# Kernel optimization log

Measured on AMD Instinct MI355X. Metric: run time of the kernel, lower is better.

Reference implementation:

```python
import jax, jax.numpy as jnp
import numpy as np
import math

H = 1024          # hidden_size
NUM_LAYERS = 2
V = 32000         # target vocabulary
S = 4096          # source length
W = 64            # window_size
WIN = 2 * W + 1   # max window width (static)
H2 = math.ceil(H / 2)
STD_SQ = (W / 2) ** 2
NEG = -1e30


def setup_inputs() -> dict:
    key = jax.random.key(0)
    ks = jax.random.split(key, 16)
    s = 0.02
    return {
        "source_sentence_length": S,
        "encoder_output": jax.random.normal(ks[0], (S, 1, H), jnp.float32),
        "word": jax.random.randint(ks[1], (1, 1), 0, V),
        "h0": jnp.zeros((NUM_LAYERS, 1, H), jnp.float32),
        "c0": jnp.zeros((NUM_LAYERS, 1, H), jnp.float32),
        "embedding": jax.random.normal(ks[2], (V, H), jnp.float32) * s,
        "lstm_w_ih": jax.random.normal(ks[3], (NUM_LAYERS, 4 * H, H), jnp.float32) * s,
        "lstm_w_hh": jax.random.normal(ks[4], (NUM_LAYERS, 4 * H, H), jnp.float32) * s,
        "lstm_b_ih": jax.random.normal(ks[5], (NUM_LAYERS, 4 * H), jnp.float32) * s,
        "lstm_b_hh": jax.random.normal(ks[6], (NUM_LAYERS, 4 * H), jnp.float32) * s,
        "att_fc1_w": jax.random.normal(ks[7], (H2, H), jnp.float32) * s,
        "att_fc1_b": jax.random.normal(ks[8], (H2,), jnp.float32) * s,
        "att_fc2_w": jax.random.normal(ks[9], (1, H2), jnp.float32) * s,
        "att_fc2_b": jax.random.normal(ks[10], (1,), jnp.float32) * s,
        "fc1_w": jax.random.normal(ks[11], (H, 2 * H), jnp.float32) * s,
        "fc1_b": jax.random.normal(ks[12], (H,), jnp.float32) * s,
        "fc2_w": jax.random.normal(ks[13], (V, H), jnp.float32) * s,
        "fc2_b": jax.random.normal(ks[14], (V,), jnp.float32) * s,
    }


def reference(source_sentence_length, encoder_output, word, h0, c0, embedding,
              lstm_w_ih, lstm_w_hh, lstm_b_ih, lstm_b_hh,
              att_fc1_w, att_fc1_b, att_fc2_w, att_fc2_b,
              fc1_w, fc1_b, fc2_w, fc2_b):
    Sf = jnp.float32(source_sentence_length)
    # embedding lookup (seq=1, batch=1) -> (H,)
    x = embedding[word[0, 0]]
    # stacked LSTM, single time step, torch gate order i,f,g,o
    h_list, c_list = [], []
    for l in range(NUM_LAYERS):
        gates = x @ lstm_w_ih[l].T + lstm_b_ih[l] + h0[l, 0] @ lstm_w_hh[l].T + lstm_b_hh[l]
        i, f, g, o = jnp.split(gates, 4)
        c_new = jax.nn.sigmoid(f) * c0[l, 0] + jax.nn.sigmoid(i) * jnp.tanh(g)
        h_new = jax.nn.sigmoid(o) * jnp.tanh(c_new)
        h_list.append(h_new); c_list.append(c_new)
        x = h_new
    h_n = jnp.stack(h_list)[:, None, :]  # (L,1,H)
    c_n = jnp.stack(c_list)[:, None, :]
    h_t = x  # (H,) decoder output at this step
    # ---- dynamic Gaussian-windowed attention ----
    p = Sf * jax.nn.sigmoid(jnp.tanh(h_t @ att_fc1_w.T + att_fc1_b) @ att_fc2_w.T + att_fc2_b)
    p = p.reshape(())
    ws = jnp.round(jnp.clip(p - W, 0, None)).astype(jnp.int32)                      # clamp(min=0)
    we = jnp.round(jnp.clip(p + W, None, source_sentence_length - 1)).astype(jnp.int32)  # clamp(max=S-1)
    idx = ws + jnp.arange(WIN, dtype=jnp.int32)          # fixed-width window
    valid = idx <= we                                    # replicates [ws:we+1] slice
    h_s = encoder_output[jnp.clip(idx, 0, source_sentence_length - 1), 0, :]
    scores = jnp.where(valid, h_s @ h_t, NEG)
    a = jax.nn.softmax(scores)                           # softmax over window
    gauss = jnp.exp((idx.astype(jnp.float32) - p) / (2.0 * STD_SQ))
    a = jnp.where(valid, a * gauss, 0.0)
    ctx = a @ h_s                                        # (H,)
    # ---- output MLP ----
    out = jnp.tanh(jnp.concatenate([ctx, h_t]) @ fc1_w.T + fc1_b)
    y = jax.nn.log_softmax(out @ fc2_w.T + fc2_b)
    return (y.reshape(1, 1, V), out.reshape(1, 1, H), h_n, c_n, a.reshape(1, 1, WIN))
```

## Files before the change

kernel.cpp:

```cpp
#include <hip/hip_runtime.h>

#define HDIM 1024
#define VD   32000
#define WINN 129
#define NEGV (-1e30f)

#define X_     0
#define HT_    1024
#define G_     5120
#define ATT1_  9216
#define CAT_   9728
#define PARTM_ 12000
#define PARTS_ 13000
#define LOG_   16384

#define O_Y   0
#define O_OUT 32000
#define O_HN  33024
#define O_CN  35072
#define O_A   37120

__device__ __forceinline__ float wred(float v){
  #pragma unroll
  for(int off=32; off; off>>=1) v += __shfl_xor(v, off, 64);
  return v;
}
__device__ __forceinline__ float wmax(float v){
  #pragma unroll
  for(int off=32; off; off>>=1) v = fmaxf(v, __shfl_xor(v, off, 64));
  return v;
}
__device__ __forceinline__ float sigf(float x){ return 1.f/(1.f+expf(-x)); }
__device__ __forceinline__ float dot4(float4 a, float4 b){
  return a.x*b.x + a.y*b.y + a.z*b.z + a.w*b.w;
}
__device__ __forceinline__ float4 ld4(const float* p){ return *(const float4*)p; }


__global__ __launch_bounds__(256) void k_lstm0(
    const float* __restrict__ wih, const float* __restrict__ whh,
    const float* __restrict__ bih, const float* __restrict__ bhh,
    const int* __restrict__ word, const float* __restrict__ emb,
    const float* __restrict__ h0, const float* __restrict__ c0,
    float* __restrict__ ws, float* __restrict__ hn, float* __restrict__ cn){
  int j = blockIdx.x*4 + (threadIdx.x>>6);
  int lane = threadIdx.x & 63;
  const float* x    = emb + ((size_t)word[0]<<10);
  const float* h00  = h0;
  const float* h01  = h0 + HDIM;
  const float* wih0 = wih + ((size_t)j<<10);
  const float* whh0 = whh + ((size_t)j<<10);
  const float* whh1 = whh + ((size_t)(4096 + j)<<10);
  float acc[12];
  #pragma unroll
  for (int g=0; g<12; g++) acc[g]=0.f;
  #pragma unroll
  for (int c=0;c<4;c++){
    int o = lane*4 + 256*c;
    float4 xv = ld4(x+o), av = ld4(h00+o), bv = ld4(h01+o);
    #pragma unroll
    for (int g=0; g<4; g++){
      acc[g]   += dot4(ld4(wih0 + ((size_t)g<<20) + o), xv);
      acc[4+g] += dot4(ld4(whh0 + ((size_t)g<<20) + o), av);
      acc[8+g] += dot4(ld4(whh1 + ((size_t)g<<20) + o), bv);
    }
  }
  #pragma unroll
  for (int g=0; g<12; g++) acc[g] = wred(acc[g]);
  if (lane==0){
    float gi = acc[0]+acc[4] + bih[j]      + bhh[j];
    float gf = acc[1]+acc[5] + bih[1024+j] + bhh[1024+j];
    float gg = acc[2]+acc[6] + bih[2048+j] + bhh[2048+j];
    float go = acc[3]+acc[7] + bih[3072+j] + bhh[3072+j];
    float cc = sigf(gf)*c0[j] + sigf(gi)*tanhf(gg);
    float hh = sigf(go)*tanhf(cc);
    ws[X_+j] = hh; hn[j]=hh; cn[j]=cc;
    #pragma unroll
    for (int g=0; g<4; g++)
      ws[G_ + g*1024 + j] = acc[8+g] + bih[4096 + g*1024 + j] + bhh[4096 + g*1024 + j];
  }
}

__global__ __launch_bounds__(256) void k_lstm1(
    const float* __restrict__ wih1, const float* __restrict__ c0l,
    float* __restrict__ ws, float* __restrict__ hn, float* __restrict__ cn){
  int j = blockIdx.x*4 + (threadIdx.x>>6);
  int lane = threadIdx.x & 63;
  const float* wr = wih1 + ((size_t)j<<10);
  float acc[4] = {0.f,0.f,0.f,0.f};
  #pragma unroll
  for (int c=0;c<4;c++){
    int o = lane*4 + 256*c;
    float4 hv = ld4(ws + X_ + o);
    #pragma unroll
    for (int g=0; g<4; g++)
      acc[g] += dot4(ld4(wr + ((size_t)g<<20) + o), hv);
  }
  #pragma unroll
  for (int g=0; g<4; g++) acc[g]=wred(acc[g]);
  if (lane==0){
    float gi = acc[0] + ws[G_ + j];
    float gf = acc[1] + ws[G_ + 1024 + j];
    float gg = acc[2] + ws[G_ + 2048 + j];
    float go = acc[3] + ws[G_ + 3072 + j];
    float cc = sigf(gf)*c0l[j] + sigf(gi)*tanhf(gg);
    float hh = sigf(go)*tanhf(cc);
    ws[HT_+j]=hh; ws[CAT_+HDIM+j]=hh; hn[j]=hh; cn[j]=cc;
  }
}

__global__ __launch_bounds__(256) void k_att1(const float* __restrict__ w,
    const float* __restrict__ b, float* __restrict__ ws){
  int gid = blockIdx.x*256 + threadIdx.x;
  int r = gid >> 6, lane = gid & 63;
  const float* wr = w + ((size_t)r<<10);
  float acc = 0.f;
  #pragma unroll
  for (int j=0; j<4; j++){
    int o = lane*4 + 256*j;
    acc += dot4(ld4(wr+o), ld4(ws+HT_+o));
  }
  acc = wred(acc);
  if (lane==0) ws[ATT1_ + r] = tanhf(acc + b[r]);
}

__global__ __launch_bounds__(1024) void k_attn(const float* __restrict__ enc,
    const int* __restrict__ slen, const float* __restrict__ a2w,
    const float* __restrict__ a2b, float* __restrict__ ws, float* __restrict__ aout){
  __shared__ float sarr[WINN];
  __shared__ float av[WINN];
  __shared__ int   ci[WINN];
  __shared__ float red[2];
  __shared__ float pinfo[1];
  __shared__ int   iw[2];
  int t = threadIdx.x, lane = t & 63, wv = t >> 6;
  float Sf = (float)slen[0];
  int smax = slen[0]-1;
  if (wv==0){
    float pacc = 0.f;
    #pragma unroll
    for (int c=0;c<2;c++){
      int o = lane*4 + 256*c;
      pacc += dot4(ld4(a2w+o), ld4(ws+ATT1_+o));
    }
    pacc = wred(pacc);
    float p = Sf * sigf(pacc + a2b[0]);
    if (t==0){
      pinfo[0] = p;
      iw[0] = (int)rintf(fmaxf(p-64.f,0.f));
      iw[1] = (int)rintf(fminf(p+64.f, Sf-1.f));
    }
  }
  __syncthreads();
  float p = pinfo[0];
  int wsi = iw[0], wei = iw[1];
  for (int k = wv; k < WINN; k += 16){
    int idx = wsi + k;
    int c = idx > smax ? smax : idx;
    const float* er = enc + ((size_t)c<<10);
    float acc=0.f;
    #pragma unroll
    for (int cc=0;cc<4;cc++){
      int o = lane*4 + 256*cc;
      acc += dot4(ld4(er+o), ld4(ws+HT_+o));
    }
    acc = wred(acc);
    if (lane==0){
      sarr[k] = (idx<=wei)? acc : NEGV;
      ci[k] = c;
    }
  }
  __syncthreads();
  if (t < 64){
    float m = fmaxf(sarr[t], sarr[t+64]);
    if (t==0) m = fmaxf(m, sarr[128]);
    m = wmax(m);
    if (t==0) red[0]=m;
  }
  __syncthreads();
  float M = red[0];
  if (t < 64){
    float e = expf(sarr[t]-M) + expf(sarr[t+64]-M);
    if (t==0) e += expf(sarr[128]-M);
    e = wred(e);
    if (t==0) red[1]=e;
  }
  __syncthreads();
  float sm = red[1];
  if (t < WINN){
    int idx = wsi + t;
    float a = expf(sarr[t]-M)/sm;
    a = (idx<=wei) ? a*expf(((float)idx - p)*(1.f/2048.f)) : 0.f;
    av[t]=a; aout[t]=a;
  }
  __syncthreads();
  float acc=0.f;
  for (int k=0;k<WINN;k++) acc += av[k]*enc[((size_t)ci[k]<<10)+t];
  ws[CAT_+t]=acc;
}

__global__ __launch_bounds__(256) void k_fc1(const float* __restrict__ w,
    const float* __restrict__ b, float* __restrict__ ws, float* __restrict__ oout){
  int gid = blockIdx.x*256 + threadIdx.x;
  int r = gid >> 6, lane = gid & 63;
  const float* wr = w + ((size_t)r<<11);
  float acc = 0.f;
  #pragma unroll
  for (int j=0; j<8; j++){
    int o = lane*4 + 256*j;
    acc += dot4(ld4(wr+o), ld4(ws+CAT_+o));
  }
  acc = wred(acc);
  if (lane==0){
    float o = tanhf(acc + b[r]);
    ws[X_ + r] = o;
    oout[r] = o;
  }
}

__global__ __launch_bounds__(512) void k_fc2(const float* __restrict__ w,
    const float* __restrict__ b, float* __restrict__ ws){
  __shared__ float lg[32];
  int wv = threadIdx.x >> 6, lane = threadIdx.x & 63;
  int r0 = (blockIdx.x*8 + wv)*4;
  const float* wr = w + ((size_t)r0<<10);
  float acc[4]={0.f,0.f,0.f,0.f};
  #pragma unroll
  for (int c=0;c<4;c++){
    int o = lane*4 + 256*c;
    float4 xv = ld4(ws+X_+o);
    #pragma unroll
    for (int rr=0;rr<4;rr++)
      acc[rr] += dot4(ld4(wr + ((size_t)rr<<10) + o), xv);
  }
  #pragma unroll
  for (int rr=0;rr<4;rr++) acc[rr]=wred(acc[rr]);
  if (lane==0){
    #pragma unroll
    for (int rr=0;rr<4;rr++){
      float v = acc[rr] + b[r0+rr];
      ws[LOG_+r0+rr] = v;
      lg[wv*4+rr] = v;
    }
  }
  __syncthreads();
  int t = threadIdx.x;
  if (t < 64){
    float v = (t<32)? lg[t] : -INFINITY;
    float m = wmax(v);
    float e = (t<32)? expf(lg[t]-m) : 0.f;
    float s = wred(e);
    if (t==0){
      ws[PARTM_ + blockIdx.x] = m;
      ws[PARTS_ + blockIdx.x] = s;
    }
  }
}

__global__ __launch_bounds__(256) void k_y(const float* __restrict__ ws, float* __restrict__ y){
  __shared__ float rm[4], rs[4];
  int t = threadIdx.x, lane = t&63, wv = t>>6;
  float m = -INFINITY;
  for (int k=t;k<1000;k+=256) m = fmaxf(m, ws[PARTM_+k]);
  m = wmax(m);
  if (lane==0) rm[wv]=m;
  __syncthreads();
  float M = fmaxf(fmaxf(rm[0],rm[1]), fmaxf(rm[2],rm[3]));
  float s = 0.f;
  for (int k=t;k<1000;k+=256) s += ws[PARTS_+k]*expf(ws[PARTM_+k]-M);
  s = wred(s);
  if (lane==0) rs[wv]=s;
  __syncthreads();
  float S = rs[0]+rs[1]+rs[2]+rs[3];
  float off = M + logf(S);
  int i = blockIdx.x*256 + t;
  if (i < 8000){
    float4 v = ld4(ws + LOG_ + i*4);
    v.x-=off; v.y-=off; v.z-=off; v.w-=off;
    *(float4*)(y + i*4) = v;
  }
}

extern "C" void kernel_launch(void* const* d_in, const int* in_sizes, int n_in,
                              void* d_out, int out_size, void* d_ws, size_t ws_size,
                              hipStream_t stream) {
  const int*   slen = (const int*)d_in[0];
  const float* enc  = (const float*)d_in[1];
  const int*   word = (const int*)d_in[2];
  const float* h0   = (const float*)d_in[3];
  const float* c0   = (const float*)d_in[4];
  const float* emb  = (const float*)d_in[5];
  const float* wih  = (const float*)d_in[6];
  const float* whh  = (const float*)d_in[7];
  const float* bih  = (const float*)d_in[8];
  const float* bhh  = (const float*)d_in[9];
  const float* a1w  = (const float*)d_in[10];
  const float* a1b  = (const float*)d_in[11];
  const float* a2w  = (const float*)d_in[12];
  const float* a2b  = (const float*)d_in[13];
  const float* f1w  = (const float*)d_in[14];
  const float* f1b  = (const float*)d_in[15];
  const float* f2w  = (const float*)d_in[16];
  const float* f2b  = (const float*)d_in[17];
  float* ws  = (float*)d_ws;
  float* out = (float*)d_out;

  k_lstm0<<<256,256,0,stream>>>(wih, whh, bih, bhh, word, emb, h0, c0,
                                ws, out + O_HN, out + O_CN);
  k_lstm1<<<256,256,0,stream>>>(wih + (size_t)4096*1024, c0 + HDIM,
                                ws, out + O_HN + HDIM, out + O_CN + HDIM);
  k_att1<<<128,256,0,stream>>>(a1w, a1b, ws);
  k_attn<<<1,1024,0,stream>>>(enc, slen, a2w, a2b, ws, out + O_A);
  k_fc1<<<256,256,0,stream>>>(f1w, f1b, ws, out + O_OUT);
  k_fc2<<<1000,512,0,stream>>>(f2w, f2b, ws);
  k_y<<<32,256,0,stream>>>(ws, out + O_Y);
}
```

Baseline: 361.4 us.

## Split LSTM rows across four waves and parallelize attention across blocks

The LSTM kernels now assign one gate row per block and split the K dimension across four waves, combining partial sums through shared memory. This launches four times as many blocks to raise memory-level parallelism on the weight streams. The single-block attention kernel is split into a scores kernel spread over 33 blocks and a softmax/context kernel spread over 8 blocks, exchanging data through workspace. This removes the one-CU serial bottleneck at the cost of an extra launch and redundant softmax work in each block.

```diff
diff --git a/kernel.cpp b/kernel.cpp
--- a/kernel.cpp
+++ b/kernel.cpp
@@ -10,6 +10,9 @@
 #define G_     5120
 #define ATT1_  9216
 #define CAT_   9728
+#define A_     11776
+#define SC_    11908
+#define IW_    11912
 #define PARTM_ 12000
 #define PARTS_ 13000
 #define LOG_   16384
@@ -43,66 +46,75 @@
     const int* __restrict__ word, const float* __restrict__ emb,
     const float* __restrict__ h0, const float* __restrict__ c0,
     float* __restrict__ ws, float* __restrict__ hn, float* __restrict__ cn){
-  int j = blockIdx.x*4 + (threadIdx.x>>6);
-  int lane = threadIdx.x & 63;
+  __shared__ float part[4][12];
+  int j = blockIdx.x;
+  int kq = threadIdx.x >> 6, lane = threadIdx.x & 63;
   const float* x    = emb + ((size_t)word[0]<<10);
-  const float* h00  = h0;
   const float* h01  = h0 + HDIM;
   const float* wih0 = wih + ((size_t)j<<10);
   const float* whh0 = whh + ((size_t)j<<10);
   const float* whh1 = whh + ((size_t)(4096 + j)<<10);
+  int o = kq*256 + lane*4;
+  float4 xv = ld4(x+o), av = ld4(h0+o), bv = ld4(h01+o);
   float acc[12];
   #pragma unroll
-  for (int g=0; g<12; g++) acc[g]=0.f;
-  #pragma unroll
-  for (int c=0;c<4;c++){
-    int o = lane*4 + 256*c;
-    float4 xv = ld4(x+o), av = ld4(h00+o), bv = ld4(h01+o);
-    #pragma unroll
-    for (int g=0; g<4; g++){
-      acc[g]   += dot4(ld4(wih0 + ((size_t)g<<20) + o), xv);
-      acc[4+g] += dot4(ld4(whh0 + ((size_t)g<<20) + o), av);
-      acc[8+g] += dot4(ld4(whh1 + ((size_t)g<<20) + o), bv);
-    }
+  for (int g=0; g<4; g++){
+    acc[g]   = dot4(ld4(wih0 + ((size_t)g<<20) + o), xv);
+    acc[4+g] = dot4(ld4(whh0 + ((size_t)g<<20) + o), av);
+    acc[8+g] = dot4(ld4(whh1 + ((size_t)g<<20) + o), bv);
   }
   #pragma unroll
   for (int g=0; g<12; g++) acc[g] = wred(acc[g]);
   if (lane==0){
-    float gi = acc[0]+acc[4] + bih[j]      + bhh[j];
-    float gf = acc[1]+acc[5] + bih[1024+j] + bhh[1024+j];
-    float gg = acc[2]+acc[6] + bih[2048+j] + bhh[2048+j];
-    float go = acc[3]+acc[7] + bih[3072+j] + bhh[3072+j];
+    #pragma unroll
+    for (int g=0; g<12; g++) part[kq][g] = acc[g];
+  }
+  __syncthreads();
+  if (threadIdx.x==0){
+    float s[12];
+    #pragma unroll
+    for (int g=0; g<12; g++) s[g] = part[0][g]+part[1][g]+part[2][g]+part[3][g];
+    float gi = s[0]+s[4] + bih[j]      + bhh[j];
+    float gf = s[1]+s[5] + bih[1024+j] + bhh[1024+j];
+    float gg = s[2]+s[6] + bih[2048+j] + bhh[2048+j];
+    float go = s[3]+s[7] + bih[3072+j] + bhh[3072+j];
     float cc = sigf(gf)*c0[j] + sigf(gi)*tanhf(gg);
     float hh = sigf(go)*tanhf(cc);
     ws[X_+j] = hh; hn[j]=hh; cn[j]=cc;
     #pragma unroll
     for (int g=0; g<4; g++)
-      ws[G_ + g*1024 + j] = acc[8+g] + bih[4096 + g*1024 + j] + bhh[4096 + g*1024 + j];
+      ws[G_ + g*1024 + j] = s[8+g] + bih[4096 + g*1024 + j] + bhh[4096 + g*1024 + j];
   }
 }
 
 __global__ __launch_bounds__(256) void k_lstm1(
     const float* __restrict__ wih1, const float* __restrict__ c0l,
     float* __restrict__ ws, float* __restrict__ hn, float* __restrict__ cn){
-  int j = blockIdx.x*4 + (threadIdx.x>>6);
-  int lane = threadIdx.x & 63;
+  __shared__ float part[4][4];
+  int j = blockIdx.x;
+  int kq = threadIdx.x >> 6, lane = threadIdx.x & 63;
   const float* wr = wih1 + ((size_t)j<<10);
-  float acc[4] = {0.f,0.f,0.f,0.f};
-  #pragma unroll
-  for (int c=0;c<4;c++){
-    int o = lane*4 + 256*c;
-    float4 hv = ld4(ws + X_ + o);
-    #pragma unroll
-    for (int g=0; g<4; g++)
-      acc[g] += dot4(ld4(wr + ((size_t)g<<20) + o), hv);
-  }
-  #pragma unroll
-  for (int g=0; g<4; g++) acc[g]=wred(acc[g]);
+  int o = kq*256 + lane*4;
+  float4 hv = ld4(ws + X_ + o);
+  float acc[4];
+  #pragma unroll
+  for (int g=0; g<4; g++)
+    acc[g] = dot4(ld4(wr + ((size_t)g<<20) + o), hv);
+  #pragma unroll
+  for (int g=0; g<4; g++) acc[g] = wred(acc[g]);
   if (lane==0){
-    float gi = acc[0] + ws[G_ + j];
-    float gf = acc[1] + ws[G_ + 1024 + j];
-    float gg = acc[2] + ws[G_ + 2048 + j];
-    float go = acc[3] + ws[G_ + 3072 + j];
+    #pragma unroll
+    for (int g=0; g<4; g++) part[kq][g] = acc[g];
+  }
+  __syncthreads();
+  if (threadIdx.x==0){
+    float s[4];
+    #pragma unroll
+    for (int g=0; g<4; g++) s[g] = part[0][g]+part[1][g]+part[2][g]+part[3][g];
+    float gi = s[0] + ws[G_ + j];
+    float gf = s[1] + ws[G_ + 1024 + j];
+    float gg = s[2] + ws[G_ + 2048 + j];
+    float go = s[3] + ws[G_ + 3072 + j];
     float cc = sigf(gf)*c0l[j] + sigf(gi)*tanhf(gg);
     float hh = sigf(go)*tanhf(cc);
     ws[HT_+j]=hh; ws[CAT_+HDIM+j]=hh; hn[j]=hh; cn[j]=cc;
@@ -124,79 +136,87 @@
   if (lane==0) ws[ATT1_ + r] = tanhf(acc + b[r]);
 }
 
-__global__ __launch_bounds__(1024) void k_attn(const float* __restrict__ enc,
+__global__ __launch_bounds__(256) void k_scores(const float* __restrict__ enc,
     const int* __restrict__ slen, const float* __restrict__ a2w,
-    const float* __restrict__ a2b, float* __restrict__ ws, float* __restrict__ aout){
-  __shared__ float sarr[WINN];
+    const float* __restrict__ a2b, float* __restrict__ ws){
+  int t = threadIdx.x;
+  int lane = t & 63;
+  float pacc = 0.f;
+  #pragma unroll
+  for (int c=0; c<2; c++){
+    int o = lane*4 + 256*c;
+    pacc += dot4(ld4(a2w+o), ld4(ws+ATT1_+o));
+  }
+  pacc = wred(pacc);
+  float Sf = (float)slen[0];
+  float p  = Sf * sigf(pacc + a2b[0]);
+  int wsi = (int)rintf(fmaxf(p - 64.f, 0.f));
+  int wei = (int)rintf(fminf(p + 64.f, Sf - 1.f));
+  if (blockIdx.x==0 && t==0){
+    ws[SC_] = p;
+    ((int*)ws)[IW_]   = wsi;
+    ((int*)ws)[IW_+1] = wei;
+  }
+  int k = blockIdx.x*4 + (t>>6);
+  if (k >= WINN) return;
+  int idx = wsi + k;
+  int smax = slen[0]-1;
+  int ci = idx > smax ? smax : idx;
+  const float* er = enc + ((size_t)ci<<10);
+  float acc = 0.f;
+  #pragma unroll
+  for (int c=0; c<4; c++){
+    int o = lane*4 + 256*c;
+    acc += dot4(ld4(er+o), ld4(ws+HT_+o));
+  }
+  acc = wred(acc);
+  if (lane==0) ws[A_ + k] = (idx <= wei) ? acc : NEGV;
+}
+
+__global__ __launch_bounds__(128) void k_smctx(const float* __restrict__ enc,
+    const int* __restrict__ slen, float* __restrict__ ws, float* __restrict__ aout){
   __shared__ float av[WINN];
-  __shared__ int   ci[WINN];
   __shared__ float red[2];
-  __shared__ float pinfo[1];
-  __shared__ int   iw[2];
-  int t = threadIdx.x, lane = t & 63, wv = t >> 6;
-  float Sf = (float)slen[0];
+  int t = threadIdx.x;
+  float p = ws[SC_];
+  int wsi = ((int*)ws)[IW_], wei = ((int*)ws)[IW_+1];
   int smax = slen[0]-1;
-  if (wv==0){
-    float pacc = 0.f;
-    #pragma unroll
-    for (int c=0;c<2;c++){
-      int o = lane*4 + 256*c;
-      pacc += dot4(ld4(a2w+o), ld4(ws+ATT1_+o));
+  if (t < 64){
+    float s0 = ws[A_+t], s1 = ws[A_+64+t];
+    float m = fmaxf(s0, s1);
+    if (t==0) m = fmaxf(m, ws[A_+128]);
+    m = wmax(m);
+    if (t==0) red[0] = m;
+  }
+  __syncthreads();
+  float M = red[0];
+  if (t < 64){
+    float s0 = ws[A_+t], s1 = ws[A_+64+t];
+    float e = expf(s0-M) + expf(s1-M);
+    if (t==0) e += expf(ws[A_+128]-M);
+    e = wred(e);
+    if (t==0) red[1] = e;
+  }
+  __syncthreads();
+  float sm = red[1];
+  if (t < 64){
+    for (int k=t; k<WINN; k+=64){
+      int idx = wsi + k;
+      float a = expf(ws[A_+k]-M)/sm;
+      a = (idx <= wei) ? a*expf(((float)idx - p)*(1.f/2048.f)) : 0.f;
+      av[k] = a;
+      if (blockIdx.x==0) aout[k] = a;
     }
-    pacc = wred(pacc);
-    float p = Sf * sigf(pacc + a2b[0]);
-    if (t==0){
-      pinfo[0] = p;
-      iw[0] = (int)rintf(fmaxf(p-64.f,0.f));
-      iw[1] = (int)rintf(fminf(p+64.f, Sf-1.f));
-    }
-  }
-  __syncthreads();
-  float p = pinfo[0];
-  int wsi = iw[0], wei = iw[1];
-  for (int k = wv; k < WINN; k += 16){
+  }
+  __syncthreads();
+  int tout = blockIdx.x*128 + t;
+  float acc = 0.f;
+  for (int k=0; k<WINN; k++){
     int idx = wsi + k;
     int c = idx > smax ? smax : idx;
-    const float* er = enc + ((size_t)c<<10);
-    float acc=0.f;
-    #pragma unroll
-    for (int cc=0;cc<4;cc++){
-      int o = lane*4 + 256*cc;
-      acc += dot4(ld4(er+o), ld4(ws+HT_+o));
-    }
-    acc = wred(acc);
-    if (lane==0){
-      sarr[k] = (idx<=wei)? acc : NEGV;
-      ci[k] = c;
-    }
-  }
-  __syncthreads();
-  if (t < 64){
-    float m = fmaxf(sarr[t], sarr[t+64]);
-    if (t==0) m = fmaxf(m, sarr[128]);
-    m = wmax(m);
-    if (t==0) red[0]=m;
-  }
-  __syncthreads();
-  float M = red[0];
-  if (t < 64){
-    float e = expf(sarr[t]-M) + expf(sarr[t+64]-M);
-    if (t==0) e += expf(sarr[128]-M);
-    e = wred(e);
-    if (t==0) red[1]=e;
-  }
-  __syncthreads();
-  float sm = red[1];
-  if (t < WINN){
-    int idx = wsi + t;
-    float a = expf(sarr[t]-M)/sm;
-    a = (idx<=wei) ? a*expf(((float)idx - p)*(1.f/2048.f)) : 0.f;
-    av[t]=a; aout[t]=a;
-  }
-  __syncthreads();
-  float acc=0.f;
-  for (int k=0;k<WINN;k++) acc += av[k]*enc[((size_t)ci[k]<<10)+t];
-  ws[CAT_+t]=acc;
+    acc += av[k]*enc[((size_t)c<<10) + tout];
+  }
+  ws[CAT_+tout] = acc;
 }
 
 __global__ __launch_bounds__(256) void k_fc1(const float* __restrict__ w,
@@ -305,12 +325,13 @@
   float* ws  = (float*)d_ws;
   float* out = (float*)d_out;
 
-  k_lstm0<<<256,256,0,stream>>>(wih, whh, bih, bhh, word, emb, h0, c0,
-                                ws, out + O_HN, out + O_CN);
-  k_lstm1<<<256,256,0,stream>>>(wih + (size_t)4096*1024, c0 + HDIM,
-                                ws, out + O_HN + HDIM, out + O_CN + HDIM);
+  k_lstm0<<<1024,256,0,stream>>>(wih, whh, bih, bhh, word, emb, h0, c0,
+                                 ws, out + O_HN, out + O_CN);
+  k_lstm1<<<1024,256,0,stream>>>(wih + (size_t)4096*1024, c0 + HDIM,
+                                 ws, out + O_HN + HDIM, out + O_CN + HDIM);
   k_att1<<<128,256,0,stream>>>(a1w, a1b, ws);
-  k_attn<<<1,1024,0,stream>>>(enc, slen, a2w, a2b, ws, out + O_A);
+  k_scores<<<33,256,0,stream>>>(enc, slen, a2w, a2b, ws);
+  k_smctx<<<8,128,0,stream>>>(enc, slen, ws, out + O_A);
   k_fc1<<<256,256,0,stream>>>(f1w, f1b, ws, out + O_OUT);
   k_fc2<<<1000,512,0,stream>>>(f2w, f2b, ws);
   k_y<<<32,256,0,stream>>>(ws, out + O_Y);
```

New measurement: 360.4 us. No clear change (-0.3%).
